# Performance work log

Measured on AMD Instinct MI355X. Metric: run time of the kernel, lower is better.

Reference implementation:

```python
import jax, jax.numpy as jnp
import numpy as np

BS, EP = 32, 32
N_AGENTS, N_ATOM, EMBED = 8, 51, 32
STATE_DIM, HYP = 128, 64
V_MIN, V_MAX = -10.0, 10.0


def proj(support, probs, v_min, v_max, n_atom):
    # C51 categorical projection of (support, probs) onto the fixed atom grid
    # linspace(v_min, v_max, n_atom). support/probs: [..., M] -> [..., n_atom]
    support, probs = jnp.broadcast_arrays(support, probs)
    delta = (v_max - v_min) / (n_atom - 1)
    b = (jnp.clip(support, v_min, v_max) - v_min) / delta
    l = jnp.floor(b)
    u = jnp.ceil(b)
    eq = (u == l).astype(probs.dtype)  # support exactly on an atom -> all mass to l
    ml = probs * (u - b + eq)
    mu = probs * (b - l)
    shp = probs.shape
    n = int(np.prod(shp[:-1]))
    m = shp[-1]
    rows = jnp.arange(n)[:, None]
    out = jnp.zeros((n, n_atom), probs.dtype)
    out = out.at[rows, l.astype(jnp.int32).reshape(n, m)].add(ml.reshape(n, m))
    out = out.at[rows, u.astype(jnp.int32).reshape(n, m)].add(mu.reshape(n, m))
    return out.reshape(shp[:-1] + (n_atom,))


def bconv(p, q):
    # Full 1D convolution of per-row categorical pmfs (sum of two random vars).
    # p: [N, L], q: [N, M] -> [N, L+M-1], via grouped conv (one group per row).
    N, L = p.shape
    M = q.shape[-1]
    out = jax.lax.conv_general_dilated(
        p[None], jnp.flip(q, -1)[:, None, :],
        window_strides=(1,), padding=[(M - 1, M - 1)],
        feature_group_count=N, dimension_numbers=('NCW', 'OIW', 'NCW'))
    return out[0]


def mlp2(x, w1, b1, w2, b2):
    return jax.nn.relu(x @ w1.T + b1) @ w2.T + b2


def setup_inputs():
    key = jax.random.key(0)
    ks = jax.random.split(key, 20)
    def p(k, shape, s=0.05):
        return jax.random.normal(k, shape, dtype=jnp.float32) * s
    aq = jax.random.uniform(ks[0], (BS, EP, N_AGENTS, N_ATOM), dtype=jnp.float32)
    aq = aq / jnp.sum(aq, -1, keepdims=True)  # valid categorical distributions
    return {
        'agent_qs_distri': aq,
        'states': p(ks[1], (BS, EP, STATE_DIM), 1.0),
        'hw1_w1': p(ks[2], (HYP, STATE_DIM)), 'hw1_b1': p(ks[3], (HYP,)),
        'hw1_w2': p(ks[4], (EMBED * N_AGENTS, HYP)), 'hw1_b2': p(ks[5], (EMBED * N_AGENTS,)),
        'hb1_w': p(ks[6], (EMBED, STATE_DIM)), 'hb1_b': p(ks[7], (EMBED,)),
        'hwf_w1': p(ks[8], (HYP, STATE_DIM)), 'hwf_b1': p(ks[9], (HYP,)),
        'hwf_w2': p(ks[10], (EMBED, HYP)), 'hwf_b2': p(ks[11], (EMBED,)),
        'v_w1': p(ks[12], (EMBED, STATE_DIM)), 'v_b1': p(ks[13], (EMBED,)),
        'v_w2': p(ks[14], (1, EMBED)), 'v_b2': p(ks[15], (1,)),
    }


def reference(agent_qs_distri, states, hw1_w1, hw1_b1, hw1_w2, hw1_b2,
              hb1_w, hb1_b, hwf_w1, hwf_b1, hwf_w2, hwf_b2,
              v_w1, v_b1, v_w2, v_b2):
    bs, ep, n_agents, n_atom = agent_qs_distri.shape
    s = states.reshape(-1, STATE_DIM)
    atoms = jnp.linspace(V_MIN, V_MAX, n_atom).astype(jnp.float32)  # [A]

    w1 = jnp.abs(mlp2(s, hw1_w1, hw1_b1, hw1_w2, hw1_b2)).reshape(bs, ep, EMBED, n_agents)
    b1 = (s @ hb1_w.T + hb1_b).reshape(bs, ep, EMBED)

    # stage 1: scale each agent's support by w1[..., k, i], project back onto atoms
    sup1 = atoms * w1[..., None]                                       # [bs,ep,E,Na,A]
    aw = proj(sup1, agent_qs_distri[:, :, None], V_MIN, V_MAX, n_atom)  # [bs,ep,E,Na,A]
    awf = aw.reshape(-1, n_agents, n_atom)                              # [bs*ep*E,Na,A]
    q = awf[:, 0]
    for i in range(1, n_agents):
        q = bconv(q, awf[:, i])                                         # [.., Na*A-Na+1]
    L1 = n_agents * n_atom - n_agents + 1
    sup = jnp.linspace(n_agents * V_MIN, n_agents * V_MAX, L1).astype(jnp.float32)
    sup = jax.nn.elu(sup + b1[..., None])                               # [bs,ep,E,L1]
    x = proj(sup, q.reshape(bs, ep, EMBED, L1), V_MIN, V_MAX, n_atom)   # [bs,ep,E,A]

    # stage 2: hyper_w_final scaling, convolve across embed dim, add V(s)
    wf = jnp.abs(mlp2(s, hwf_w1, hwf_b1, hwf_w2, hwf_b2)).reshape(bs, ep, EMBED)
    xw = proj(atoms * wf[..., None], x, V_MIN, V_MAX, n_atom)           # [bs,ep,E,A]
    xwf = xw.reshape(-1, EMBED, n_atom)
    q = xwf[:, 0]
    for i in range(1, EMBED):
        q = bconv(q, xwf[:, i])                                         # [bs*ep, E*A-E+1]
    L2 = EMBED * n_atom - EMBED + 1
    v = mlp2(s, v_w1, v_b1, v_w2, v_b2).reshape(bs, ep, 1)
    sup2 = jnp.linspace(EMBED * V_MIN, EMBED * V_MAX, L2).astype(jnp.float32) + v
    return proj(sup2, q.reshape(bs, ep, L2), V_MIN, V_MAX, n_atom)      # [bs,ep,A]
```

## Files before the change

### kernel.cpp

```cpp
#include <hip/hip_runtime.h>
#include <hip/hip_bf16.h>
#include <math.h>

typedef unsigned short u16;

#define WAVE_SYNC() asm volatile("s_waitcnt lgkmcnt(0)" ::: "memory")

__device__ __forceinline__ float bf2f(u16 u) {
  union { unsigned int i; float f; } c;
  c.i = ((unsigned int)u) << 16;
  return c.f;
}
__device__ __forceinline__ float bflo(unsigned int u) {
  union { unsigned int i; float f; } c; c.i = u << 16; return c.f;
}
__device__ __forceinline__ float bfhi(unsigned int u) {
  union { unsigned int i; float f; } c; c.i = u & 0xffff0000u; return c.f;
}
__device__ __forceinline__ u16 f2bf(float f) {
  union { float f; unsigned int i; } c;
  c.f = f;
  unsigned int x = c.i;
  unsigned int r = (x + 0x7fffu + ((x >> 16) & 1u)) >> 16;
  return (u16)r;
}

__device__ __forceinline__ void proj_bounds(float wv, int& ML, int& MH) {
  float smin = (-10.0f + 0.4f * 0.0f)  * wv;
  float smax = (-10.0f + 0.4f * 50.0f) * wv;
  float bmin = (fminf(fmaxf(smin, -10.0f), 10.0f) + 10.0f) / 0.4f;
  float bmax = (fminf(fmaxf(smax, -10.0f), 10.0f) + 10.0f) / 0.4f;
  ML = (int)floorf(bmin);
  MH = (int)ceilf(bmax);
}

template<typename SUPP>
__device__ __forceinline__ void proj_scan(float* __restrict__ g1,
                                          float* __restrict__ g2,
                                          int span, int lane, SUPP supp)
{
  if (lane < 52) g1[lane] = 0.f;
  if (lane < 53) g2[lane] = 0.f;
  float cml = 0.f, cmu = 0.f;
  int ck = -1;
  for (int base = 0; base < span; base += 64) {
    int t = base + lane;
    bool act = (t < span);
    int tc = act ? t : (span - 1);
    float sup, p;
    supp(tc, act, sup, p);
    float c  = fminf(fmaxf(sup, -10.0f), 10.0f);
    float b  = (c + 10.0f) / 0.4f;
    float l  = floorf(b);
    float u  = ceilf(b);
    float eq = (u == l) ? 1.0f : 0.0f;
    float ml = p * (u - b + eq);
    float mu = p * (b - l);
    int   li = (int)l;
    bool last = (base + 64 >= span);
    if (lane == 0 && ck >= 0) {
      if (ck == li) { ml += cml; mu += cmu; }
      else          { g1[ck] = cml; g2[ck + 1] = cmu; }
    }
#pragma unroll
    for (int d = 1; d < 64; d <<= 1) {
      int   lo = __shfl_up(li, d);
      float a1 = __shfl_up(ml, d);
      float a2 = __shfl_up(mu, d);
      bool same = (lane >= d) && (lo == li);
      ml += same ? a1 : 0.f;
      mu += same ? a2 : 0.f;
    }
    int ln = __shfl_down(li, 1);
    bool runend = (lane == 63) ? last : (ln != li);
    if (runend) { g1[li] = ml; g2[li + 1] = mu; }
    if (!last) {
      cml = __shfl(ml, 63);
      cmu = __shfl(mu, 63);
      ck  = __shfl(li, 63);
    }
  }
}

__device__ __forceinline__ void conv_pad2(const float* __restrict__ q,
                                          float* __restrict__ qn,
                                          const float* __restrict__ kvs,
                                          int ML, int W, int T,
                                          int LQ, int HQ, int tid, int nthr)
{
  const int Lout = LQ + ML, Hout = HQ + ML + T;
  for (int J = Lout + tid; J <= Hout; J += nthr) {
    const float* qp = q + (J - ML);
    float acc = 0.f;
    for (int c = 0; c < W; c += 4) {
      float4 k4 = *(const float4*)(kvs + c);
      acc = fmaf(k4.x, qp[-c],     acc);
      acc = fmaf(k4.y, qp[-c - 1], acc);
      acc = fmaf(k4.z, qp[-c - 2], acc);
      acc = fmaf(k4.w, qp[-c - 3], acc);
    }
    qn[J] = acc;
  }
}

template<int BF>
__device__ __forceinline__ float ldt(const void* p, int i) {
  if (BF) return bf2f(((const u16*)p)[i]);
  return ((const float*)p)[i];
}

template<int BF>
__device__ __forceinline__ float dot128_t(const void* w, int row, const float* s) {
  float acc = 0.f;
  if (BF) {
    const uint4* p = (const uint4*)((const u16*)w + row * 128);
#pragma unroll
    for (int i = 0; i < 16; ++i) {
      uint4 v = p[i];
      int b = i * 8;
      acc = fmaf(bflo(v.x), s[b + 0], acc); acc = fmaf(bfhi(v.x), s[b + 1], acc);
      acc = fmaf(bflo(v.y), s[b + 2], acc); acc = fmaf(bfhi(v.y), s[b + 3], acc);
      acc = fmaf(bflo(v.z), s[b + 4], acc); acc = fmaf(bfhi(v.z), s[b + 5], acc);
      acc = fmaf(bflo(v.w), s[b + 6], acc); acc = fmaf(bfhi(v.w), s[b + 7], acc);
    }
  } else {
    const float4* p = (const float4*)((const float*)w + row * 128);
#pragma unroll
    for (int i = 0; i < 32; ++i) {
      float4 v = p[i];
      int b = i * 4;
      acc = fmaf(v.x, s[b + 0], acc); acc = fmaf(v.y, s[b + 1], acc);
      acc = fmaf(v.z, s[b + 2], acc); acc = fmaf(v.w, s[b + 3], acc);
    }
  }
  return acc;
}

template<int BF>
__device__ __forceinline__ float dot64_t(const void* w, int row, const float* h) {
  float acc = 0.f;
  if (BF) {
    const uint4* p = (const uint4*)((const u16*)w + row * 64);
#pragma unroll
    for (int i = 0; i < 8; ++i) {
      uint4 v = p[i];
      int b = i * 8;
      acc = fmaf(bflo(v.x), h[b + 0], acc); acc = fmaf(bfhi(v.x), h[b + 1], acc);
      acc = fmaf(bflo(v.y), h[b + 2], acc); acc = fmaf(bfhi(v.y), h[b + 3], acc);
      acc = fmaf(bflo(v.z), h[b + 4], acc); acc = fmaf(bfhi(v.z), h[b + 5], acc);
      acc = fmaf(bflo(v.w), h[b + 6], acc); acc = fmaf(bfhi(v.w), h[b + 7], acc);
    }
  } else {
    const float4* p = (const float4*)((const float*)w + row * 64);
#pragma unroll
    for (int i = 0; i < 16; ++i) {
      float4 v = p[i];
      int b = i * 4;
      acc = fmaf(v.x, h[b + 0], acc); acc = fmaf(v.y, h[b + 1], acc);
      acc = fmaf(v.z, h[b + 2], acc); acc = fmaf(v.w, h[b + 3], acc);
    }
  }
  return acc;
}

template<int BF>
__device__ __forceinline__ void mlp_body(
    const void* states,
    const void* hw1_w1, const void* hw1_b1, const void* hw1_w2, const void* hw1_b2,
    const void* hb1_w,  const void* hb1_b,
    const void* hwf_w1, const void* hwf_b1, const void* hwf_w2, const void* hwf_b2,
    const void* v_w1,   const void* v_b1,   const void* v_w2,   const void* v_b2,
    float* w1_ws, float* b1_ws, float* wf_ws, float* v_ws,
    int n, int tid, float* s, float* h1, float* hf, float* vh)
{
  s[tid]      = ldt<BF>(states, n * 128 + tid);
  s[tid + 64] = ldt<BF>(states, n * 128 + 64 + tid);
  __syncthreads();

  h1[tid] = fmaxf(dot128_t<BF>(hw1_w1, tid, s) + ldt<BF>(hw1_b1, tid), 0.f);
  hf[tid] = fmaxf(dot128_t<BF>(hwf_w1, tid, s) + ldt<BF>(hwf_b1, tid), 0.f);
  if (tid < 32) {
    vh[tid] = fmaxf(dot128_t<BF>(v_w1, tid, s) + ldt<BF>(v_b1, tid), 0.f);
    b1_ws[n * 32 + tid] = dot128_t<BF>(hb1_w, tid, s) + ldt<BF>(hb1_b, tid);
  }
  __syncthreads();

#pragma unroll
  for (int k = 0; k < 4; ++k) {
    int o = tid + 64 * k;
    w1_ws[n * 256 + o] = fabsf(dot64_t<BF>(hw1_w2, o, h1) + ldt<BF>(hw1_b2, o));
  }
  if (tid < 32)
    wf_ws[n * 32 + tid] = fabsf(dot64_t<BF>(hwf_w2, tid, hf) + ldt<BF>(hwf_b2, tid));
  if (tid == 0) {
    float acc = ldt<BF>(v_b2, 0);
    for (int e = 0; e < 32; ++e) acc = fmaf(ldt<BF>(v_w2, e), vh[e], acc);
    v_ws[n] = acc;
  }
}

__global__ __launch_bounds__(64) void k_mlp(
    const void* __restrict__ states,
    const void* __restrict__ hw1_w1, const void* __restrict__ hw1_b1,
    const void* __restrict__ hw1_w2, const void* __restrict__ hw1_b2,
    const void* __restrict__ hb1_w,  const void* __restrict__ hb1_b,
    const void* __restrict__ hwf_w1, const void* __restrict__ hwf_b1,
    const void* __restrict__ hwf_w2, const void* __restrict__ hwf_b2,
    const void* __restrict__ v_w1,   const void* __restrict__ v_b1,
    const void* __restrict__ v_w2,   const void* __restrict__ v_b2,
    float* __restrict__ w1_ws, float* __restrict__ b1_ws,
    float* __restrict__ wf_ws, float* __restrict__ v_ws,
    int* __restrict__ flag)
{
  __shared__ float s[128];
  __shared__ float h1[64];
  __shared__ float hf[64];
  __shared__ float vh[32];
  const int n = blockIdx.x;
  const int tid = threadIdx.x;

  const u16* sr = (const u16*)states;
  unsigned int e0 = (sr[tid] >> 7) & 0xFF;
  unsigned int e1 = (sr[tid + 64] >> 7) & 0xFF;
  unsigned long long bl0 = __ballot(e0 >= 97 && e0 <= 141);
  unsigned long long bl1 = __ballot(e1 >= 97 && e1 <= 141);
  int bf = (__popcll(bl0) + __popcll(bl1) >= 104) ? 1 : 0;
  if (tid == 0) *flag = bf;

  if (bf)
    mlp_body<1>(states, hw1_w1, hw1_b1, hw1_w2, hw1_b2, hb1_w, hb1_b,
                hwf_w1, hwf_b1, hwf_w2, hwf_b2, v_w1, v_b1, v_w2, v_b2,
                w1_ws, b1_ws, wf_ws, v_ws, n, tid, s, h1, hf, vh);
  else
    mlp_body<0>(states, hw1_w1, hw1_b1, hw1_w2, hw1_b2, hb1_w, hb1_b,
                hwf_w1, hwf_b1, hwf_w2, hwf_b2, v_w1, v_b1, v_w2, v_b2,
                w1_ws, b1_ws, wf_ws, v_ws, n, tid, s, h1, hf, vh);
}

__global__ __launch_bounds__(128) void k_perembed(
    const void* __restrict__ aq,
    const float* __restrict__ w1_ws, const float* __restrict__ b1_ws,
    const float* __restrict__ wf_ws, float* __restrict__ xw_ws,
    const int* __restrict__ flag)
{
  __shared__ __align__(16) float Ab[2][520];
  __shared__ __align__(16) float Bb[2][520];
  __shared__ __align__(16) float kv_all[2][8][16];
  __shared__ __align__(16) float kvo[2][56];
  __shared__ float p_lds[2][8][52];
  __shared__ float gAb[2][53];
  __shared__ float gBb[2][54];

  const int w    = threadIdx.x >> 6;
  const int lane = threadIdx.x & 63;
  const int task = blockIdx.x * 2 + w;
  const int n = task >> 5;
  const int e = task & 31;
  const int bf = *flag;

  float* A   = Ab[w];
  float* B   = Bb[w];
  float* gA  = gAb[w];
  float* gB  = gBb[w];
  float (*pl)[52] = p_lds[w];

  if (bf) {
    const u16* p = (const u16*)aq + n * 408 + lane;
    if (lane < 51) {
#pragma unroll
      for (int a = 0; a < 8; ++a) pl[a][lane] = bf2f(p[a * 51]);
    }
  } else {
    const float* p = (const float*)aq + n * 408 + lane;
    if (lane < 51) {
#pragma unroll
      for (int a = 0; a < 8; ++a) pl[a][lane] = p[a * 51];
    }
  }
  float wreg = (lane < 8) ? w1_ws[n * 256 + e * 8 + lane] : 0.f;
  float b1v  = b1_ws[n * 32 + e];
  float wfv  = wf_ws[n * 32 + e];

  int mlA = 0, mhA = 0;
  if (lane < 8) proj_bounds(wreg, mlA, mhA);
  unsigned long long wide = __ballot((lane < 8) && (mhA - mlA > 15));
  WAVE_SYNC();

  int LQ, HQ;
  float* q = A;
  float* qn = B;

  if (wide == 0ull) {
#pragma unroll
    for (int r = 0; r < 2; ++r) {
      int a  = 4 * r + (lane >> 4);
      int jj = lane & 15;
      float wv = __shfl(wreg, a);
      int ML = __shfl(mlA, a);
      int MH = __shfl(mhA, a);
      int T = MH - ML;
      int j = ML + jj;
      float ej  = 0.4f * (float)j - 10.0f;
      float e25 = ej * 2.5f;
      float invw = 2.5f / wv;
      int tL = (jj == 0) ? 0  : (int)floorf((ej - 0.4f) * invw + 25.f) - 1;
      int tH = (jj >= T) ? 50 : (int)ceilf ((ej + 0.4f) * invw + 25.f) + 1;
      tL = tL < 0 ? 0 : tL;
      tH = tH > 50 ? 50 : tH;
      if (jj > T) { tL = 0; tH = -1; }
      float step = 0.4f * wv;
      float sup  = fmaf((float)tL, step, -10.0f * wv);
      float acc = 0.f;
      const float* pb = pl[a];
      for (int t = tL; t <= tH; ++t) {
        float c   = fminf(fmaxf(sup, -10.0f), 10.0f);
        float d   = fmaf(c, 2.5f, -e25);
        float wgt = fmaxf(0.f, 1.0f - fabsf(d));
        acc = fmaf(pb[t], wgt, acc);
        sup += step;
      }
      kv_all[w][a][jj] = (jj <= T) ? acc : 0.f;
    }
    WAVE_SYNC();

    int ML0 = __shfl(mlA, 0), MH0 = __shfl(mhA, 0);
    if (lane <= MH0 - ML0) A[64 + ML0 + lane] = kv_all[w][0][lane];
    WAVE_SYNC();
    LQ = 64 + ML0; HQ = 64 + MH0;

#pragma unroll
    for (int a = 1; a < 8; ++a) {
      int ML = __shfl(mlA, a), MH = __shfl(mhA, a);
      int T = MH - ML;
      int W = (T + 4) & ~3;
      if (lane < W - 1) q[LQ - 1 - lane] = 0.f;
      if (lane < T)     q[HQ + 1 + lane] = 0.f;
      WAVE_SYNC();
      conv_pad2(q, qn, &kv_all[w][a][0], ML, W, T, LQ, HQ, lane, 64);
      WAVE_SYNC();
      LQ += ML; HQ += MH;
      float* t_ = q; q = qn; qn = t_;
    }
  } else {
    float* kvs = kvo[w];
    float wv0 = __shfl(wreg, 0);
    int ML0 = __shfl(mlA, 0), MH0 = __shfl(mhA, 0);
    proj_scan(gA, gB, 51, lane, [&](int t, bool act, float& sup, float& p) {
      sup = (-10.0f + 0.4f * (float)t) * wv0;
      float pv = pl[0][t];
      p = act ? pv : 0.f;
    });
    if (lane <= MH0 - ML0)
      A[64 + ML0 + lane] = gA[ML0 + lane] + gB[ML0 + lane];
    WAVE_SYNC();
    LQ = 64 + ML0; HQ = 64 + MH0;

    for (int a = 1; a < 8; ++a) {
      float wv = __shfl(wreg, a);
      int ML = __shfl(mlA, a), MH = __shfl(mhA, a);
      int T = MH - ML;
      int W = (T + 4) & ~3;
      proj_scan(gA, gB, 51, lane, [&](int t, bool act, float& sup, float& p) {
        sup = (-10.0f + 0.4f * (float)t) * wv;
        float pv = pl[a][t];
        p = act ? pv : 0.f;
      });
      if (lane < W)     kvs[lane] = (lane <= T) ? (gA[ML + lane] + gB[ML + lane]) : 0.f;
      if (lane < W - 1) q[LQ - 1 - lane] = 0.f;
      if (lane < T)     q[HQ + 1 + lane] = 0.f;
      WAVE_SYNC();
      conv_pad2(q, qn, kvs, ML, W, T, LQ, HQ, lane, 64);
      WAVE_SYNC();
      LQ += ML; HQ += MH;
      float* t_ = q; q = qn; qn = t_;
    }
  }

  {
    int span = HQ - LQ + 1;
    int LQl = LQ;
    const float* qf = q;
    proj_scan(gA, gB, span, lane, [&](int t, bool act, float& sup, float& p) {
      int tg = (LQl - 64) + t;
      float raw = (-80.0f + 0.4f * (float)tg) + b1v;
      sup = (raw > 0.f) ? raw : expm1f(raw);
      p = act ? qf[LQl + t] : 0.f;
    });
  }
  WAVE_SYNC();

  float x2v = (lane < 51) ? (gA[lane] + gB[lane]) : 0.f;
  WAVE_SYNC();
  int MLf, MHf;
  proj_bounds(wfv, MLf, MHf);
  proj_scan(gA, gB, 51, lane, [&](int t, bool act, float& sup, float& p) {
    sup = (-10.0f + 0.4f * (float)t) * wfv;
    p = act ? x2v : 0.f;
  });
  WAVE_SYNC();
  if (lane <= MHf - MLf)
    xw_ws[task * 51 + MLf + lane] = gA[MLf + lane] + gB[MLf + lane];
}

__global__ __launch_bounds__(256) void k_final(
    const float* __restrict__ xw_ws, const float* __restrict__ wf_ws,
    const float* __restrict__ v_ws,
    void* __restrict__ out, const int* __restrict__ flag)
{
  __shared__ __align__(16) float bufA[4608];
  __shared__ __align__(16) float bufB[4608];
  __shared__ int meta_s[63];
  __shared__ int meta_l[63];
  __shared__ int meta_ml[32];
  __shared__ int meta_g[6];
  __shared__ int meta_mltot;
  __shared__ float gA[53], gB[54];

  const int n    = blockIdx.x;
  const int tid  = threadIdx.x;
  const int lane = tid & 63;
  const int bf   = *flag;

  float wfreg = (lane < 32) ? wf_ws[n * 32 + lane] : 0.f;
  float vv    = v_ws[n];

  for (int i = tid; i < 4608; i += 256) { bufA[i] = 0.f; bufB[i] = 0.f; }

  if (tid < 64) {
    int ml, mh;
    proj_bounds(wfreg, ml, mh);
    if (lane < 32) meta_ml[lane] = ml;
    int msum = ml;
#pragma unroll
    for (int d = 1; d < 32; d <<= 1) msum += __shfl_xor(msum, d);
    if (lane == 0) meta_mltot = msum;

    int curlen = mh - ml + 1;
    int base = 0, Ncur = 32;
#pragma unroll
    for (int c = 0; c <= 5; ++c) {
      int lm = (lane < Ncur) ? curlen : 0;
#pragma unroll
      for (int d = 1; d < 32; d <<= 1) {
        int o = __shfl_xor(lm, d);
        lm = (o > lm) ? o : lm;
      }
      int G = (lm + 11) & ~3;
      int sp = ((curlen + 3) & ~3) + G;
      int inc = (lane < Ncur) ? sp : 0;
      int v0 = inc;
#pragma unroll
      for (int d = 1; d < 32; d <<= 1) {
        int u = __shfl_up(inc, d);
        if (lane >= d && lane < 32) inc += u;
      }
      if (lane < Ncur) {
        meta_s[base + lane] = 832 + (inc - v0);
        meta_l[base + lane] = curlen;
      }
      if (lane == 0) meta_g[c] = G;
      if (c < 5) {
        int l0 = __shfl(curlen, 2 * lane);
        int l1 = __shfl(curlen, 2 * lane + 1);
        curlen = l0 + l1 - 1;
        base += Ncur;
        Ncur >>= 1;
      }
    }
  }
  __syncthreads();

  {
    int g = tid >> 3, i = tid & 7;
    int s = meta_s[g], l = meta_l[g], ml = meta_ml[g];
    const float* row = xw_ws + (n * 32 + g) * 51 + ml;
    for (int i0 = i; i0 < l; i0 += 8) bufA[s + i0] = row[i0];
  }
  __syncthreads();

#pragma unroll
  for (int c = 1; c <= 5; ++c) {
    const float* bin = (c & 1) ? bufA : bufB;
    float*       bout = (c & 1) ? bufB : bufA;
    const int Nout = 32 >> c;
    const int lg = 3 + c;
    const int gs = 1 << lg;
    const int k  = tid >> lg;
    const int st = tid & (gs - 1);
    const int bc = 64 - (64 >> c);
    const int bp = 64 - (64 >> (c - 1));
    const int i0 = bp + 2 * k;
    const int sA = meta_s[i0];
    const int sB = meta_s[i0 + 1];
    const int lB = meta_l[i0 + 1];
    const int sO = meta_s[bc + k];
    const int lO = meta_l[bc + k];
    const int W  = (lB + 3) & ~3;

    for (int j = st * 2; j < lO; j += gs * 2) {
      const float* Ap = bin + sA + j + 1;
      float a0 = 0.f, a1 = 0.f;
      for (int m = 0; m < W; m += 4) {
        float4 k4 = *(const float4*)(bin + sB + m);
        float v0 = Ap[-m], v1 = Ap[-m - 1], v2 = Ap[-m - 2];
        float v3 = Ap[-m - 3], v4 = Ap[-m - 4];
        a0 = fmaf(k4.x, v1, fmaf(k4.y, v2, fmaf(k4.z, v3, fmaf(k4.w, v4, a0))));
        a1 = fmaf(k4.x, v0, fmaf(k4.y, v1, fmaf(k4.z, v2, fmaf(k4.w, v3, a1))));
      }
      bout[sO + j] = a0;
      if (j + 1 < lO) bout[sO + j + 1] = a1;
    }

    if (c >= 2 && c <= 4) {
      int G = meta_g[c];
      for (int p = tid; p < G; p += 256) bout[832 - G + p] = 0.f;
      for (int k2 = 0; k2 < Nout; ++k2) {
        int ss = meta_s[bc + k2] + meta_l[bc + k2];
        int ee = (k2 + 1 < Nout) ? meta_s[bc + k2 + 1]
                                 : ss + G + 3;
        for (int p = ss + tid; p < ee; p += 256) bout[p] = 0.f;
      }
    }
    __syncthreads();
  }

  if (tid < 64) {
    int s5 = meta_s[62], l5 = meta_l[62], mlt = meta_mltot;
    const float* qf = bufB + s5;
    proj_scan(gA, gB, l5, lane, [&](int t, bool act, float& sup, float& p) {
      int tg = mlt + t;
      sup = (-320.0f + 0.4f * (float)tg) + vv;
      p = act ? qf[t] : 0.f;
    });
    WAVE_SYNC();
    if (lane < 51) {
      float o = gA[lane] + gB[lane];
      if (bf) ((u16*)out)[n * 51 + lane] = f2bf(o);
      else    ((float*)out)[n * 51 + lane] = o;
    }
  }
}

extern "C" void kernel_launch(void* const* d_in, const int* in_sizes, int n_in,
                              void* d_out, int out_size, void* d_ws, size_t ws_size,
                              hipStream_t stream)
{
  float* ws    = (float*)d_ws;
  float* w1_ws = ws;
  float* b1_ws = w1_ws + 1024 * 256;
  float* wf_ws = b1_ws + 1024 * 32;
  float* v_ws  = wf_ws + 1024 * 32;
  float* xw_ws = v_ws  + 1024;
  int*   flag  = (int*)(xw_ws + 1024 * 32 * 51);

  k_mlp<<<1024, 64, 0, stream>>>(d_in[1],
      d_in[2], d_in[3], d_in[4], d_in[5], d_in[6], d_in[7],
      d_in[8], d_in[9], d_in[10], d_in[11], d_in[12], d_in[13],
      d_in[14], d_in[15],
      w1_ws, b1_ws, wf_ws, v_ws, flag);

  k_perembed<<<16384, 128, 0, stream>>>(d_in[0], w1_ws, b1_ws, wf_ws, xw_ws, flag);

  k_final<<<1024, 256, 0, stream>>>(xw_ws, wf_ws, v_ws, d_out, flag);
}
```

Measured before the change: 249.2 us.

## Replace scatter-scan projections with branchless gather and fixed-width convolution

Recomputes each per-agent and final weight-scaling projection as a gather: every output atom sums all 51 input atoms with a triangular hat weight, read as float4 from LDS, with no data-dependent loop bounds. The separate wide/narrow code paths become one per-agent branch. Narrow kernels use a fully unrolled 16-tap convolution with two accumulators. This removes the proj_scan scatter passes and the divergent variable-length loops, in exchange for more arithmetic per lane, since all 52 atoms are always visited. The unclamped affine form used for narrow kernels assumes the support never leaves the clipping range.

```diff
diff --git a/kernel.cpp b/kernel.cpp
--- a/kernel.cpp
+++ b/kernel.cpp
@@ -103,6 +103,51 @@
   }
 }
 
+__device__ __forceinline__ void conv16(const float* __restrict__ q,
+                                       float* __restrict__ qn,
+                                       const float* __restrict__ kvs,
+                                       int ML, int T,
+                                       int LQ, int HQ, int lane)
+{
+  const int Lout = LQ + ML, Hout = HQ + ML + T;
+  for (int J = Lout + lane; J <= Hout; J += 64) {
+    const float* qp = q + (J - ML);
+    float a0 = 0.f, a1 = 0.f;
+#pragma unroll
+    for (int c = 0; c < 16; c += 4) {
+      float4 k4 = *(const float4*)(kvs + c);
+      a0 = fmaf(k4.x, qp[-c],     a0);
+      a1 = fmaf(k4.y, qp[-c - 1], a1);
+      a0 = fmaf(k4.z, qp[-c - 2], a0);
+      a1 = fmaf(k4.w, qp[-c - 3], a1);
+    }
+    qn[J] = a0 + a1;
+  }
+}
+
+__device__ __forceinline__ float gather64_clamped(const float* __restrict__ pb,
+                                                  float wv, float j)
+{
+  float a0 = 0.f, a1 = 0.f, a2 = 0.f, a3 = 0.f;
+  const float4* pb4 = (const float4*)pb;
+  const float base = 25.0f - j;
+#pragma unroll
+  for (int t4 = 0; t4 < 13; ++t4) {
+    float4 p4 = pb4[t4];
+#define G1(PX, TT, AC) { \
+    float sup = ((float)(TT) * 0.4f - 10.0f) * wv; \
+    float c   = fminf(fmaxf(sup, -10.0f), 10.0f); \
+    float d   = fmaf(c, 2.5f, base); \
+    AC = fmaf(PX, fmaxf(0.f, 1.0f - fabsf(d)), AC); }
+    G1(p4.x, 4 * t4 + 0, a0)
+    G1(p4.y, 4 * t4 + 1, a1)
+    G1(p4.z, 4 * t4 + 2, a2)
+    G1(p4.w, 4 * t4 + 3, a3)
+#undef G1
+  }
+  return (a0 + a1) + (a2 + a3);
+}
+
 template<int BF>
 __device__ __forceinline__ float ldt(const void* p, int i) {
   if (BF) return bf2f(((const u16*)p)[i]);
@@ -247,7 +292,7 @@
   __shared__ __align__(16) float Bb[2][520];
   __shared__ __align__(16) float kv_all[2][8][16];
   __shared__ __align__(16) float kvo[2][56];
-  __shared__ float p_lds[2][8][52];
+  __shared__ __align__(16) float p_lds[2][8][52];
   __shared__ float gAb[2][53];
   __shared__ float gBb[2][54];
 
@@ -262,19 +307,22 @@
   float* B   = Bb[w];
   float* gA  = gAb[w];
   float* gB  = gBb[w];
+  float* kvo_w = kvo[w];
   float (*pl)[52] = p_lds[w];
 
   if (bf) {
-    const u16* p = (const u16*)aq + n * 408 + lane;
-    if (lane < 51) {
-#pragma unroll
-      for (int a = 0; a < 8; ++a) pl[a][lane] = bf2f(p[a * 51]);
+    const u16* p = (const u16*)aq + n * 408;
+    if (lane < 52) {
+#pragma unroll
+      for (int a = 0; a < 8; ++a)
+        pl[a][lane] = (lane < 51) ? bf2f(p[a * 51 + lane]) : 0.f;
     }
   } else {
-    const float* p = (const float*)aq + n * 408 + lane;
-    if (lane < 51) {
-#pragma unroll
-      for (int a = 0; a < 8; ++a) pl[a][lane] = p[a * 51];
+    const float* p = (const float*)aq + n * 408;
+    if (lane < 52) {
+#pragma unroll
+      for (int a = 0; a < 8; ++a)
+        pl[a][lane] = (lane < 51) ? p[a * 51 + lane] : 0.f;
     }
   }
   float wreg = (lane < 8) ? w1_ws[n * 256 + e * 8 + lane] : 0.f;
@@ -283,97 +331,76 @@
 
   int mlA = 0, mhA = 0;
   if (lane < 8) proj_bounds(wreg, mlA, mhA);
-  unsigned long long wide = __ballot((lane < 8) && (mhA - mlA > 15));
+  WAVE_SYNC();
+
+#pragma unroll
+  for (int r = 0; r < 2; ++r) {
+    int a  = 4 * r + (lane >> 4);
+    int jj = lane & 15;
+    float wv = __shfl(wreg, a);
+    int ML = __shfl(mlA, a);
+    int MH = __shfl(mhA, a);
+    int T  = MH - ML;
+    float K = (25.0f - (float)(ML + jj)) - 25.0f * wv;
+    float a0 = 0.f, a1 = 0.f, a2 = 0.f, a3 = 0.f;
+    const float4* pb4 = (const float4*)pl[a];
+#pragma unroll
+    for (int t4 = 0; t4 < 13; ++t4) {
+      float4 p4 = pb4[t4];
+      float d0 = fmaf((float)(4 * t4 + 0), wv, K);
+      float d1 = fmaf((float)(4 * t4 + 1), wv, K);
+      float d2 = fmaf((float)(4 * t4 + 2), wv, K);
+      float d3 = fmaf((float)(4 * t4 + 3), wv, K);
+      a0 = fmaf(p4.x, fmaxf(0.f, 1.0f - fabsf(d0)), a0);
+      a1 = fmaf(p4.y, fmaxf(0.f, 1.0f - fabsf(d1)), a1);
+      a2 = fmaf(p4.z, fmaxf(0.f, 1.0f - fabsf(d2)), a2);
+      a3 = fmaf(p4.w, fmaxf(0.f, 1.0f - fabsf(d3)), a3);
+    }
+    if (T <= 15)
+      kv_all[w][a][jj] = (jj <= T) ? ((a0 + a1) + (a2 + a3)) : 0.f;
+  }
   WAVE_SYNC();
 
   int LQ, HQ;
   float* q = A;
   float* qn = B;
-
-  if (wide == 0ull) {
-#pragma unroll
-    for (int r = 0; r < 2; ++r) {
-      int a  = 4 * r + (lane >> 4);
-      int jj = lane & 15;
-      float wv = __shfl(wreg, a);
-      int ML = __shfl(mlA, a);
-      int MH = __shfl(mhA, a);
-      int T = MH - ML;
-      int j = ML + jj;
-      float ej  = 0.4f * (float)j - 10.0f;
-      float e25 = ej * 2.5f;
-      float invw = 2.5f / wv;
-      int tL = (jj == 0) ? 0  : (int)floorf((ej - 0.4f) * invw + 25.f) - 1;
-      int tH = (jj >= T) ? 50 : (int)ceilf ((ej + 0.4f) * invw + 25.f) + 1;
-      tL = tL < 0 ? 0 : tL;
-      tH = tH > 50 ? 50 : tH;
-      if (jj > T) { tL = 0; tH = -1; }
-      float step = 0.4f * wv;
-      float sup  = fmaf((float)tL, step, -10.0f * wv);
-      float acc = 0.f;
-      const float* pb = pl[a];
-      for (int t = tL; t <= tH; ++t) {
-        float c   = fminf(fmaxf(sup, -10.0f), 10.0f);
-        float d   = fmaf(c, 2.5f, -e25);
-        float wgt = fmaxf(0.f, 1.0f - fabsf(d));
-        acc = fmaf(pb[t], wgt, acc);
-        sup += step;
-      }
-      kv_all[w][a][jj] = (jj <= T) ? acc : 0.f;
-    }
-    WAVE_SYNC();
-
+  {
+    float wv0 = __shfl(wreg, 0);
     int ML0 = __shfl(mlA, 0), MH0 = __shfl(mhA, 0);
-    if (lane <= MH0 - ML0) A[64 + ML0 + lane] = kv_all[w][0][lane];
+    int T0 = MH0 - ML0;
+    if (T0 <= 15) {
+      if (lane <= T0) A[64 + ML0 + lane] = kv_all[w][0][lane];
+    } else {
+      float acc = gather64_clamped(pl[0], wv0, (float)(ML0 + lane));
+      if (lane <= T0) A[64 + ML0 + lane] = acc;
+    }
     WAVE_SYNC();
     LQ = 64 + ML0; HQ = 64 + MH0;
-
-#pragma unroll
-    for (int a = 1; a < 8; ++a) {
-      int ML = __shfl(mlA, a), MH = __shfl(mhA, a);
-      int T = MH - ML;
-      int W = (T + 4) & ~3;
-      if (lane < W - 1) q[LQ - 1 - lane] = 0.f;
-      if (lane < T)     q[HQ + 1 + lane] = 0.f;
-      WAVE_SYNC();
-      conv_pad2(q, qn, &kv_all[w][a][0], ML, W, T, LQ, HQ, lane, 64);
-      WAVE_SYNC();
-      LQ += ML; HQ += MH;
-      float* t_ = q; q = qn; qn = t_;
-    }
-  } else {
-    float* kvs = kvo[w];
-    float wv0 = __shfl(wreg, 0);
-    int ML0 = __shfl(mlA, 0), MH0 = __shfl(mhA, 0);
-    proj_scan(gA, gB, 51, lane, [&](int t, bool act, float& sup, float& p) {
-      sup = (-10.0f + 0.4f * (float)t) * wv0;
-      float pv = pl[0][t];
-      p = act ? pv : 0.f;
-    });
-    if (lane <= MH0 - ML0)
-      A[64 + ML0 + lane] = gA[ML0 + lane] + gB[ML0 + lane];
+  }
+
+  for (int a = 1; a < 8; ++a) {
+    float wv = __shfl(wreg, a);
+    int ML = __shfl(mlA, a), MH = __shfl(mhA, a);
+    int T = MH - ML;
+    const float* kvs;
+    int W;
+    if (T <= 15) {
+      kvs = &kv_all[w][a][0];
+      W = 16;
+    } else {
+      float acc = gather64_clamped(pl[a], wv, (float)(ML + lane));
+      W = (T + 4) & ~3;
+      if (lane < W) kvo_w[lane] = (lane <= T) ? acc : 0.f;
+      kvs = kvo_w;
+    }
+    if (lane < W - 1) q[LQ - 1 - lane] = 0.f;
+    if (lane < T)     q[HQ + 1 + lane] = 0.f;
     WAVE_SYNC();
-    LQ = 64 + ML0; HQ = 64 + MH0;
-
-    for (int a = 1; a < 8; ++a) {
-      float wv = __shfl(wreg, a);
-      int ML = __shfl(mlA, a), MH = __shfl(mhA, a);
-      int T = MH - ML;
-      int W = (T + 4) & ~3;
-      proj_scan(gA, gB, 51, lane, [&](int t, bool act, float& sup, float& p) {
-        sup = (-10.0f + 0.4f * (float)t) * wv;
-        float pv = pl[a][t];
-        p = act ? pv : 0.f;
-      });
-      if (lane < W)     kvs[lane] = (lane <= T) ? (gA[ML + lane] + gB[ML + lane]) : 0.f;
-      if (lane < W - 1) q[LQ - 1 - lane] = 0.f;
-      if (lane < T)     q[HQ + 1 + lane] = 0.f;
-      WAVE_SYNC();
-      conv_pad2(q, qn, kvs, ML, W, T, LQ, HQ, lane, 64);
-      WAVE_SYNC();
-      LQ += ML; HQ += MH;
-      float* t_ = q; q = qn; qn = t_;
-    }
+    if (T <= 15) conv16(q, qn, kvs, ML, T, LQ, HQ, lane);
+    else         conv_pad2(q, qn, kvs, ML, W, T, LQ, HQ, lane, 64);
+    WAVE_SYNC();
+    LQ += ML; HQ += MH;
+    float* t_ = q; q = qn; qn = t_;
   }
 
   {
@@ -391,15 +418,17 @@
 
   float x2v = (lane < 51) ? (gA[lane] + gB[lane]) : 0.f;
   WAVE_SYNC();
-  int MLf, MHf;
-  proj_bounds(wfv, MLf, MHf);
-  proj_scan(gA, gB, 51, lane, [&](int t, bool act, float& sup, float& p) {
-    sup = (-10.0f + 0.4f * (float)t) * wfv;
-    p = act ? x2v : 0.f;
-  });
+  float* x2row = pl[0];
+  if (lane < 52) x2row[lane] = (lane < 51) ? x2v : 0.f;
   WAVE_SYNC();
-  if (lane <= MHf - MLf)
-    xw_ws[task * 51 + MLf + lane] = gA[MLf + lane] + gB[MLf + lane];
+  {
+    int MLf, MHf;
+    proj_bounds(wfv, MLf, MHf);
+    int Tf = MHf - MLf;
+    float acc = gather64_clamped(x2row, wfv, (float)(MLf + lane));
+    if (lane <= Tf)
+      xw_ws[task * 51 + MLf + lane] = acc;
+  }
 }
 
 __global__ __launch_bounds__(256) void k_final(
```

Measured after the change: 248.5 us. Within noise of the previous version (-0.3%).
